# Optimization experiments

Measured on AMD Instinct MI355X. Metric: run time of the kernel, lower is better.

## Reference

```python
import jax, jax.numpy as jnp
import numpy as np

N = 50000
NUM_USERS = 20000
E = 800000
IN_DIM = 256
OUT_DIM = 256
H = 8
DK = OUT_DIM // H


def setup_inputs() -> dict:
    key = jax.random.key(0)
    ks = jax.random.split(key, 16)
    inp = {
        "x": jax.random.normal(ks[0], (N, IN_DIM), dtype=jnp.float32),
        "row": jax.random.randint(ks[1], (E,), 0, N, dtype=jnp.int32),
        "col": jax.random.randint(ks[2], (E,), 0, N, dtype=jnp.int32),
        "relation_emb": jax.random.normal(ks[3], (OUT_DIM,), dtype=jnp.float32),
        "user_text_embs": jax.random.normal(ks[4], (NUM_USERS, IN_DIM), dtype=jnp.float32),
        "item_text_embs": jax.random.normal(ks[5], (N - NUM_USERS, IN_DIM), dtype=jnp.float32),
        "Wq": jax.random.normal(ks[6], (OUT_DIM, IN_DIM), dtype=jnp.float32) * 0.02,
        "bq": jnp.zeros((OUT_DIM,), dtype=jnp.float32),
        "Wk": jax.random.normal(ks[7], (OUT_DIM, IN_DIM), dtype=jnp.float32) * 0.02,
        "bk": jnp.zeros((OUT_DIM,), dtype=jnp.float32),
        "Wv": jax.random.normal(ks[8], (OUT_DIM, IN_DIM), dtype=jnp.float32) * 0.02,
        "bv": jnp.zeros((OUT_DIM,), dtype=jnp.float32),
        "Wo": jax.random.normal(ks[9], (OUT_DIM, OUT_DIM), dtype=jnp.float32) * 0.02,
        "bo": jnp.zeros((OUT_DIM,), dtype=jnp.float32),
    }
    return inp


def reference(x, row, col, relation_emb, user_text_embs, item_text_embs,
              Wq, bq, Wk, bk, Wv, bv, Wo, bo):
    # text_emb: users first, then items (matches torch zeros_like + slice assign)
    text_emb = jnp.concatenate([user_text_embs, item_text_embs], axis=0)  # [N, in_dim]

    Q = (text_emb @ Wq.T + bq).reshape(N, H, DK)
    K = (text_emb @ Wk.T + bk).reshape(N, H, DK)
    V = (x @ Wv.T + bv).reshape(N, H, DK)

    Q_ = Q[col]  # [E, H, DK]
    K_ = K[row]
    V_ = V[row]
    rel = relation_emb.reshape(1, H, DK)

    scores = jnp.sum(Q_ * (K_ + rel), axis=-1) / np.sqrt(DK).astype(np.float32)  # [E, H]

    # segment softmax over destination node (col)
    m = jax.ops.segment_max(scores, col, num_segments=N)          # [N, H]
    e = jnp.exp(scores - m[col])                                   # [E, H]
    denom = jax.ops.segment_sum(e, col, num_segments=N)           # [N, H]
    attn = e / denom[col]                                          # [E, H]

    out = jax.ops.segment_sum(attn[:, :, None] * V_, col, num_segments=N)  # [N, H, DK]
    out = out.reshape(N, OUT_DIM)
    return out @ Wo.T + bo
```

## Files before the change

kernel.cpp:

```cpp
#include <hip/hip_runtime.h>
#include <hip/hip_bf16.h>

#define N_NODES   50000
#define N_USERS   20000
#define N_EDGES   800000
#define DIM       256
#define NHEAD     8
#define DKH       32
#define NBLK_SCAN ((N_NODES + 255) / 256)
#define NGRP_PAD  3128
#define NBLK_HIST ((N_EDGES + 255) / 256)
#define NBLK_G64  (NGRP_PAD / 4)
#define KVROW     768

typedef __attribute__((ext_vector_type(8))) short bf16x8;
typedef __attribute__((ext_vector_type(4))) float f32x4;
typedef __attribute__((ext_vector_type(4))) unsigned short u16x4;
typedef __attribute__((ext_vector_type(8))) unsigned short u16x8;

__device__ inline unsigned short f2bf(float f) {
    union { __hip_bfloat16 b; unsigned short u; } cv;
    cv.b = __float2bfloat16(f);
    return cv.u;
}
__device__ inline float bf2f(unsigned short u) {
    return __uint_as_float(((unsigned int)u) << 16);
}
__device__ inline unsigned char f2fp8(float f) {
    unsigned int p = __builtin_amdgcn_cvt_pk_fp8_f32(f, f, 0, false);
    return (unsigned char)(p & 0xff);
}


__global__ void prep_kernel(const float* __restrict__ Wq, const float* __restrict__ Wk,
                            const float* __restrict__ Wv, const float* __restrict__ Wo,
                            unsigned short* __restrict__ Wb2,
                            const int* __restrict__ col, int* __restrict__ cnt,
                            int* __restrict__ erank)
{
    int b = blockIdx.x;
    if (b < 128) {
        int gid = b * 256 + threadIdx.x;
        const float* srcs[4] = { Wq, Wk, Wv, Wo };
        int m = gid >> 13, slot = gid & 8191;
        int lane = slot & 63, ks = (slot >> 6) & 7, g = slot >> 9;
        int c = g * 16 + (lane & 15);
        int d = ks * 32 + (lane >> 4) * 8;
        const float* s = srcs[m] + (size_t)c * DIM + d;
        float4 f0 = *(const float4*)s, f1 = *(const float4*)(s + 4);
        u16x8 o = { f2bf(f0.x), f2bf(f0.y), f2bf(f0.z), f2bf(f0.w),
                    f2bf(f1.x), f2bf(f1.y), f2bf(f1.z), f2bf(f1.w) };
        *(u16x8*)(Wb2 + (size_t)m * 65536 + (size_t)slot * 8) = o;
    } else {
        int e = (b - 128) * 256 + threadIdx.x;
        if (e < N_EDGES) erank[e] = atomicAdd(&cnt[col[e]], 1);
    }
}

__device__ __forceinline__ void stage_a_lds(const float* __restrict__ Alo,
                                            const float* __restrict__ Ahi,
                                            int split, int row0, int M,
                                            unsigned short* Asm, int tid)
{
    const int w = tid >> 6, lane = tid & 63;
    #pragma unroll
    for (int it = 0; it < 8; ++it) {
        int f = it * 4 + w;
        int g = f >> 3, ks = f & 7;
        int r = g * 16 + (lane & 15);
        int d = ks * 32 + (lane >> 4) * 8;
        int ga = row0 + r; if (ga >= M) ga = M - 1;
        const float* src = ((ga < split) ? Alo + (size_t)ga * DIM
                                         : Ahi + (size_t)(ga - split) * DIM) + d;
        float4 f0 = *(const float4*)src, f1 = *(const float4*)(src + 4);
        u16x8 hv = { f2bf(f0.x), f2bf(f0.y), f2bf(f0.z), f2bf(f0.w),
                     f2bf(f1.x), f2bf(f1.y), f2bf(f1.z), f2bf(f1.w) };
        *(u16x8*)((char*)Asm + (size_t)f * 1024 + lane * 16) = hv;
    }
}

__device__ __forceinline__ void mfma_core_lds(const unsigned short* Asm,
                                              const unsigned short* __restrict__ W2,
                                              f32x4 acc[2][8], int lane, int wid)
{
    const int gAl = (wid >> 1) * 2;
    const int gB = (wid & 1) * 8;
    #pragma unroll
    for (int ks = 0; ks < 8; ++ks) {
        bf16x8 a[2], b[8];
        #pragma unroll
        for (int i = 0; i < 2; ++i)
            a[i] = *(const bf16x8*)((const char*)Asm + (size_t)((gAl + i) * 8 + ks) * 1024 + lane * 16);
        #pragma unroll
        for (int j = 0; j < 8; ++j)
            b[j] = *(const bf16x8*)(W2 + (size_t)((gB + j) * 8 + ks) * 512 + lane * 8);
        #pragma unroll
        for (int i = 0; i < 2; ++i)
            #pragma unroll
            for (int j = 0; j < 8; ++j)
                acc[i][j] = __builtin_amdgcn_mfma_f32_16x16x32_bf16(a[i], b[j], acc[i][j], 0, 0, 0);
    }
}

__device__ __forceinline__ void mfma_core64(const unsigned short* __restrict__ A2,
                                            const unsigned short* __restrict__ W2,
                                            int row0, f32x4 acc[2][8],
                                            int lane, int wid)
{
    const int gA = (row0 >> 4) + (wid >> 1) * 2;
    const int gB = (wid & 1) * 8;
    #pragma unroll
    for (int ks = 0; ks < 8; ++ks) {
        bf16x8 a[2], b[8];
        #pragma unroll
        for (int i = 0; i < 2; ++i)
            a[i] = *(const bf16x8*)(A2 + (size_t)((gA + i) * 8 + ks) * 512 + lane * 8);
        #pragma unroll
        for (int j = 0; j < 8; ++j)
            b[j] = *(const bf16x8*)(W2 + (size_t)((gB + j) * 8 + ks) * 512 + lane * 8);
        #pragma unroll
        for (int i = 0; i < 2; ++i)
            #pragma unroll
            for (int j = 0; j < 8; ++j)
                acc[i][j] = __builtin_amdgcn_mfma_f32_16x16x32_bf16(a[i], b[j], acc[i][j], 0, 0, 0);
    }
}

template<int MODE>
__device__ __forceinline__ void epilogue64(f32x4 acc[2][8], const float* bias, void* Cv,
                                           int row0, int M, int lane, int wid)
{
    const int wm = wid >> 1, wn = wid & 1;
    const int lr = lane & 15, lk = lane >> 4;
    float* Cf = (float*)Cv;
    unsigned short* Cb = (unsigned short*)Cv;
    unsigned char* C8 = (unsigned char*)Cv;
    #pragma unroll
    for (int i = 0; i < 2; ++i) {
        #pragma unroll
        for (int r = 0; r < 4; ++r) {
            int grow = row0 + wm * 32 + i * 16 + lk * 4 + r;
            if (grow >= M) continue;
            #pragma unroll
            for (int j = 0; j < 8; ++j) {
                int gcol = wn * 128 + j * 16 + lr;
                float val = acc[i][j][r] + bias[gcol];
                if constexpr (MODE == 0) {
                    Cf[(size_t)grow * 256 + gcol] = val;
                } else if constexpr (MODE == 1) {
                    Cb[(size_t)grow * 256 + gcol] = f2bf(val);
                } else if constexpr (MODE == 2) {
                    C8[(size_t)grow * KVROW + gcol] = f2fp8(val);
                } else {
                    *(unsigned short*)(C8 + (size_t)grow * KVROW + 256 + gcol * 2) = f2bf(val);
                }
            }
        }
    }
}

__global__ __launch_bounds__(256) void gemm_qkv_scatter(
    const float* __restrict__ user, const float* __restrict__ item,
    const float* __restrict__ x,
    const unsigned short* __restrict__ Wb2,
    const float* __restrict__ bq, const float* __restrict__ bk, const float* __restrict__ bv,
    unsigned short* __restrict__ Qb, unsigned char* __restrict__ KVb, int M,
    const int* __restrict__ row, const int* __restrict__ col,
    const int* __restrict__ erank, const int* __restrict__ offs,
    int* __restrict__ esrc)
{
    const int b = blockIdx.x;
    if (b < NBLK_HIST) {
        int e = b * 256 + threadIdx.x;
        if (e < N_EDGES) {
            int c = col[e];
            esrc[offs[c] + erank[e]] = row[e];
        }
        return;
    }
    __shared__ unsigned short Asm[64 * 256];
    const int gb = b - NBLK_HIST;
    const int isv = gb >= NBLK_G64;
    const int row0 = (isv ? gb - NBLK_G64 : gb) * 64;
    const int tid = threadIdx.x;
    const int lane = tid & 63, wid = tid >> 6;

    if (isv) stage_a_lds(x, x, M, row0, M, Asm, tid);
    else     stage_a_lds(user, item, N_USERS, row0, M, Asm, tid);
    __syncthreads();

    f32x4 acc[2][8];
    if (isv) {
        #pragma unroll
        for (int i = 0; i < 2; ++i)
            #pragma unroll
            for (int j = 0; j < 8; ++j) acc[i][j] = (f32x4){0.f, 0.f, 0.f, 0.f};
        mfma_core_lds(Asm, Wb2 + 2 * 65536, acc, lane, wid);
        epilogue64<3>(acc, bv, KVb, row0, M, lane, wid);
    } else {
        #pragma unroll
        for (int i = 0; i < 2; ++i)
            #pragma unroll
            for (int j = 0; j < 8; ++j) acc[i][j] = (f32x4){0.f, 0.f, 0.f, 0.f};
        mfma_core_lds(Asm, Wb2, acc, lane, wid);
        epilogue64<1>(acc, bq, Qb, row0, M, lane, wid);
        #pragma unroll
        for (int i = 0; i < 2; ++i)
            #pragma unroll
            for (int j = 0; j < 8; ++j) acc[i][j] = (f32x4){0.f, 0.f, 0.f, 0.f};
        mfma_core_lds(Asm, Wb2 + 65536, acc, lane, wid);
        epilogue64<2>(acc, bk, KVb, row0, M, lane, wid);
    }
}

__global__ __launch_bounds__(256) void gemm_o_reg(
    const unsigned short* __restrict__ A2,
    const unsigned short* __restrict__ Wb2, const float* __restrict__ bo,
    float* __restrict__ C, int M)
{
    const int tid = threadIdx.x;
    const int lane = tid & 63, wid = tid >> 6;
    const int row0 = blockIdx.x * 64;

    f32x4 acc[2][8];
    #pragma unroll
    for (int i = 0; i < 2; ++i)
        #pragma unroll
        for (int j = 0; j < 8; ++j) acc[i][j] = (f32x4){0.f, 0.f, 0.f, 0.f};

    mfma_core64(A2, Wb2 + 3 * 65536, row0, acc, lane, wid);
    epilogue64<0>(acc, bo, C, row0, M, lane, wid);
}

__global__ __launch_bounds__(256) void scan_blk_kernel(const int* __restrict__ cnt,
                                                       int* __restrict__ offs_tmp,
                                                       int* __restrict__ bsum) {
    __shared__ int s[256];
    int b = blockIdx.x, t = threadIdx.x;
    int i = b * 256 + t;
    int v = (i < N_NODES) ? cnt[i] : 0;
    s[t] = v;
    __syncthreads();
    #pragma unroll
    for (int d = 1; d < 256; d <<= 1) {
        int u = (t >= d) ? s[t - d] : 0;
        __syncthreads();
        s[t] += u;
        __syncthreads();
    }
    if (i < N_NODES) offs_tmp[i] = s[t] - v;
    if (t == 255) bsum[b] = s[255];
}

__global__ __launch_bounds__(256) void scan_top_kernel(int* __restrict__ bsum) {
    __shared__ int s[256];
    int t = threadIdx.x;
    int v = (t < NBLK_SCAN) ? bsum[t] : 0;
    s[t] = v;
    __syncthreads();
    #pragma unroll
    for (int d = 1; d < 256; d <<= 1) {
        int u = (t >= d) ? s[t - d] : 0;
        __syncthreads();
        s[t] += u;
        __syncthreads();
    }
    if (t < NBLK_SCAN) bsum[t] = s[t] - v;
}

__global__ __launch_bounds__(256) void scan_add_kernel(const int* __restrict__ offs_tmp,
                                                       const int* __restrict__ bsum,
                                                       int* __restrict__ offs) {
    int i = blockIdx.x * 256 + threadIdx.x;
    if (i == 0) offs[N_NODES] = N_EDGES;
    if (i >= N_NODES) return;
    offs[i] = offs_tmp[i] + bsum[blockIdx.x];
}

__global__ __launch_bounds__(256) void node_fused_kernel(
    const unsigned short* __restrict__ Qb, const unsigned char* __restrict__ KVb,
    const float* __restrict__ rel,
    const int* __restrict__ offs, const int* __restrict__ esrc,
    unsigned short* __restrict__ outagg2)
{
    const float SC = 0.17677669529663687f;
    int wid = (blockIdx.x * blockDim.x + threadIdx.x) >> 6;
    int lane = threadIdx.x & 63;
    if (wid >= N_NODES) return;
    int beg = offs[wid], end = offs[wid + 1];
    int d0 = lane * 4;
    const unsigned char* kbase = KVb + lane * 4;
    const unsigned char* vbase = KVb + 256 + lane * 8;

    u16x4 qb4 = *(const u16x4*)(Qb + (size_t)wid * DIM + d0);
    float qx = bf2f(qb4[0]), qy = bf2f(qb4[1]), qz = bf2f(qb4[2]), qw = bf2f(qb4[3]);
    float4 rl = *(const float4*)(rel + d0);

    float p0 = qx * rl.x + qy * rl.y + qz * rl.z + qw * rl.w;
    p0 += __shfl_xor(p0, 1);
    p0 += __shfl_xor(p0, 2);
    p0 += __shfl_xor(p0, 4);

    float den = 0.f;
    float4 acc = make_float4(0.f, 0.f, 0.f, 0.f);

    for (int base = beg; base < end; base += 64) {
        int n = end - base; if (n > 64) n = 64;
        int idx = base + lane; if (idx >= end) idx = end - 1;
        int my = esrc[idx];
        int j = 0;
        for (; j + 8 <= n; j += 8) {
            unsigned int kw[8]; u16x4 vv[8];
            #pragma unroll
            for (int u = 0; u < 8; ++u) {
                int r = __shfl(my, j + u);
                size_t ro = (size_t)r * KVROW;
                kw[u] = *(const unsigned int*)(kbase + ro);
                vv[u] = *(const u16x4*)(vbase + ro);
            }
            float s[8];
            #pragma unroll
            for (int u = 0; u < 8; ++u)
                s[u] = qx * __builtin_amdgcn_cvt_f32_fp8(kw[u], 0)
                     + qy * __builtin_amdgcn_cvt_f32_fp8(kw[u], 1)
                     + qz * __builtin_amdgcn_cvt_f32_fp8(kw[u], 2)
                     + qw * __builtin_amdgcn_cvt_f32_fp8(kw[u], 3);
            #pragma unroll
            for (int u = 0; u < 8; ++u) {
                s[u] += __shfl_xor(s[u], 1);
                s[u] += __shfl_xor(s[u], 2);
                s[u] += __shfl_xor(s[u], 4);
            }
            #pragma unroll
            for (int u = 0; u < 8; ++u) {
                float w = __expf((s[u] + p0) * SC);
                den += w;
                acc.x += w * bf2f(vv[u][0]); acc.y += w * bf2f(vv[u][1]);
                acc.z += w * bf2f(vv[u][2]); acc.w += w * bf2f(vv[u][3]);
            }
        }
        for (; j + 4 <= n; j += 4) {
            unsigned int kw[4]; u16x4 vv[4];
            #pragma unroll
            for (int u = 0; u < 4; ++u) {
                int r = __shfl(my, j + u);
                size_t ro = (size_t)r * KVROW;
                kw[u] = *(const unsigned int*)(kbase + ro);
                vv[u] = *(const u16x4*)(vbase + ro);
            }
            float s[4];
            #pragma unroll
            for (int u = 0; u < 4; ++u)
                s[u] = qx * __builtin_amdgcn_cvt_f32_fp8(kw[u], 0)
                     + qy * __builtin_amdgcn_cvt_f32_fp8(kw[u], 1)
                     + qz * __builtin_amdgcn_cvt_f32_fp8(kw[u], 2)
                     + qw * __builtin_amdgcn_cvt_f32_fp8(kw[u], 3);
            #pragma unroll
            for (int u = 0; u < 4; ++u) {
                s[u] += __shfl_xor(s[u], 1);
                s[u] += __shfl_xor(s[u], 2);
                s[u] += __shfl_xor(s[u], 4);
            }
            #pragma unroll
            for (int u = 0; u < 4; ++u) {
                float w = __expf((s[u] + p0) * SC);
                den += w;
                acc.x += w * bf2f(vv[u][0]); acc.y += w * bf2f(vv[u][1]);
                acc.z += w * bf2f(vv[u][2]); acc.w += w * bf2f(vv[u][3]);
            }
        }
        for (; j < n; ++j) {
            int r = __shfl(my, j);
            size_t ro = (size_t)r * KVROW;
            unsigned int kw = *(const unsigned int*)(kbase + ro);
            u16x4 vv = *(const u16x4*)(vbase + ro);
            float s0 = qx * __builtin_amdgcn_cvt_f32_fp8(kw, 0)
                     + qy * __builtin_amdgcn_cvt_f32_fp8(kw, 1)
                     + qz * __builtin_amdgcn_cvt_f32_fp8(kw, 2)
                     + qw * __builtin_amdgcn_cvt_f32_fp8(kw, 3);
            s0 += __shfl_xor(s0, 1);
            s0 += __shfl_xor(s0, 2);
            s0 += __shfl_xor(s0, 4);
            float w0 = __expf((s0 + p0) * SC);
            den += w0;
            acc.x += w0 * bf2f(vv[0]); acc.y += w0 * bf2f(vv[1]);
            acc.z += w0 * bf2f(vv[2]); acc.w += w0 * bf2f(vv[3]);
        }
    }
    float rden = (end > beg) ? 1.f / den : 0.f;
    u16x4 o = { f2bf(acc.x * rden), f2bf(acc.y * rden),
                f2bf(acc.z * rden), f2bf(acc.w * rden) };
    int ks = lane >> 3, lk = (lane >> 1) & 3, e4 = (lane & 1) * 4;
    size_t toff = ((size_t)(wid >> 4) * 8 + ks) * 512 + (lk * 16 + (wid & 15)) * 8 + e4;
    *(u16x4*)(outagg2 + toff) = o;
}

extern "C" void kernel_launch(void* const* d_in, const int* in_sizes, int n_in,
                              void* d_out, int out_size, void* d_ws, size_t ws_size,
                              hipStream_t stream) {
    const float* x    = (const float*)d_in[0];
    const int*   row  = (const int*)d_in[1];
    const int*   col  = (const int*)d_in[2];
    const float* rel  = (const float*)d_in[3];
    const float* user = (const float*)d_in[4];
    const float* item = (const float*)d_in[5];
    const float* Wq   = (const float*)d_in[6];
    const float* bq   = (const float*)d_in[7];
    const float* Wk   = (const float*)d_in[8];
    const float* bk   = (const float*)d_in[9];
    const float* Wv   = (const float*)d_in[10];
    const float* bv   = (const float*)d_in[11];
    const float* Wo   = (const float*)d_in[12];
    const float* bo   = (const float*)d_in[13];

    char* ws = (char*)d_ws;
    size_t off = 0;
    auto alloc = [&](size_t bytes) -> void* {
        void* p = ws + off;
        off = (off + bytes + 255) & ~(size_t)255;
        return p;
    };
    const size_t tiled_sz = (size_t)NGRP_PAD * 4096 * 2;
    unsigned short* Qb      = (unsigned short*)alloc((size_t)N_NODES * DIM * 2);
    unsigned char*  KVb     = (unsigned char*)alloc((size_t)N_NODES * KVROW);
    unsigned short* outagg2 = (unsigned short*)alloc(tiled_sz);
    unsigned short* Wb2     = (unsigned short*)alloc((size_t)4 * 65536 * 2);
    int*   cnt      = (int*)alloc((size_t)N_NODES * 4);
    int*   offs     = (int*)alloc((size_t)(N_NODES + 1) * 4);
    int*   offs_tmp = (int*)alloc((size_t)N_NODES * 4);
    int*   bsum     = (int*)alloc((size_t)NBLK_SCAN * 4);
    int*   esrc     = (int*)alloc((size_t)N_EDGES * 4);
    int*   erank    = (int*)alloc((size_t)N_EDGES * 4);

    hipMemsetAsync(cnt, 0, (size_t)N_NODES * 4, stream);

    prep_kernel<<<128 + NBLK_HIST, 256, 0, stream>>>(
        Wq, Wk, Wv, Wo, Wb2, col, cnt, erank);
    scan_blk_kernel<<<NBLK_SCAN, 256, 0, stream>>>(cnt, offs_tmp, bsum);
    scan_top_kernel<<<1, 256, 0, stream>>>(bsum);
    scan_add_kernel<<<NBLK_SCAN, 256, 0, stream>>>(offs_tmp, bsum, offs);

    gemm_qkv_scatter<<<NBLK_HIST + 2 * NBLK_G64, 256, 0, stream>>>(
        user, item, x, Wb2, bq, bk, bv, Qb, KVb, N_NODES,
        row, col, erank, offs, esrc);

    node_fused_kernel<<<(N_NODES * 64 + 255) / 256, 256, 0, stream>>>(
        Qb, KVb, rel, offs, esrc, outagg2);

    gemm_o_reg<<<NBLK_G64, 256, 0, stream>>>(outagg2, Wb2, bo, (float*)d_out, N_NODES);
}
```

Measured before the change: 231.1 us.

## Interleave scatter and QKV GEMM blocks, split Q/K into separate blocks

The fused launch now interleaves blocks in groups of seven: four edge-scatter blocks and three GEMM blocks covering Q, K and V for the same 64-row tile. Previously all scatter blocks ran first and each Q/K block did two GEMMs in sequence. Splitting Q and K into their own blocks balances per-block work. Interleaving mixes memory-bound scatter work with compute-bound MFMA work across the GPU. The cost is that each user/item A tile is now staged into LDS twice, once by the Q block and once by the K block.

```diff
diff --git a/kernel.cpp b/kernel.cpp
--- a/kernel.cpp
+++ b/kernel.cpp
@@ -170,8 +170,9 @@
     int* __restrict__ esrc)
 {
     const int b = blockIdx.x;
-    if (b < NBLK_HIST) {
-        int e = b * 256 + threadIdx.x;
+    const int grp = b / 7, rem = b % 7;
+    if (rem < 4) {
+        int e = (grp * 4 + rem) * 256 + threadIdx.x;
         if (e < N_EDGES) {
             int c = col[e];
             esrc[offs[c] + erank[e]] = row[e];
@@ -179,38 +180,26 @@
         return;
     }
     __shared__ unsigned short Asm[64 * 256];
-    const int gb = b - NBLK_HIST;
-    const int isv = gb >= NBLK_G64;
-    const int row0 = (isv ? gb - NBLK_G64 : gb) * 64;
+    const int mat = rem - 4;
+    const int row0 = grp * 64;
     const int tid = threadIdx.x;
     const int lane = tid & 63, wid = tid >> 6;
 
-    if (isv) stage_a_lds(x, x, M, row0, M, Asm, tid);
-    else     stage_a_lds(user, item, N_USERS, row0, M, Asm, tid);
+    if (mat == 2) stage_a_lds(x, x, M, row0, M, Asm, tid);
+    else          stage_a_lds(user, item, N_USERS, row0, M, Asm, tid);
     __syncthreads();
 
     f32x4 acc[2][8];
-    if (isv) {
-        #pragma unroll
-        for (int i = 0; i < 2; ++i)
-            #pragma unroll
-            for (int j = 0; j < 8; ++j) acc[i][j] = (f32x4){0.f, 0.f, 0.f, 0.f};
-        mfma_core_lds(Asm, Wb2 + 2 * 65536, acc, lane, wid);
-        epilogue64<3>(acc, bv, KVb, row0, M, lane, wid);
-    } else {
-        #pragma unroll
-        for (int i = 0; i < 2; ++i)
-            #pragma unroll
-            for (int j = 0; j < 8; ++j) acc[i][j] = (f32x4){0.f, 0.f, 0.f, 0.f};
-        mfma_core_lds(Asm, Wb2, acc, lane, wid);
-        epilogue64<1>(acc, bq, Qb, row0, M, lane, wid);
-        #pragma unroll
-        for (int i = 0; i < 2; ++i)
-            #pragma unroll
-            for (int j = 0; j < 8; ++j) acc[i][j] = (f32x4){0.f, 0.f, 0.f, 0.f};
-        mfma_core_lds(Asm, Wb2 + 65536, acc, lane, wid);
-        epilogue64<2>(acc, bk, KVb, row0, M, lane, wid);
-    }
+    #pragma unroll
+    for (int i = 0; i < 2; ++i)
+        #pragma unroll
+        for (int j = 0; j < 8; ++j) acc[i][j] = (f32x4){0.f, 0.f, 0.f, 0.f};
+
+    mfma_core_lds(Asm, Wb2 + (size_t)mat * 65536, acc, lane, wid);
+
+    if (mat == 0)      epilogue64<1>(acc, bq, Qb,  row0, M, lane, wid);
+    else if (mat == 1) epilogue64<2>(acc, bk, KVb, row0, M, lane, wid);
+    else               epilogue64<3>(acc, bv, KVb, row0, M, lane, wid);
 }
 
 __global__ __launch_bounds__(256) void gemm_o_reg(
@@ -440,7 +429,7 @@
     scan_top_kernel<<<1, 256, 0, stream>>>(bsum);
     scan_add_kernel<<<NBLK_SCAN, 256, 0, stream>>>(offs_tmp, bsum, offs);
 
-    gemm_qkv_scatter<<<NBLK_HIST + 2 * NBLK_G64, 256, 0, stream>>>(
+    gemm_qkv_scatter<<<7 * NBLK_G64, 256, 0, stream>>>(
         user, item, x, Wb2, bq, bk, bv, Qb, KVb, N_NODES,
         row, col, erank, offs, esrc);
 
```

Result: no change. 231.4 us (+0.1%).
